# Kernel optimization log

Hardware: AMD Instinct MI355X
Metric: run time of the kernel (lower is better)

The kernel has to match this reference:

```python
import jax, jax.numpy as jnp
import numpy as np

B, S, D, H = 2, 2048, 2048, 16
HD = D // H


def setup_inputs() -> dict:
    key = jax.random.key(0)
    ks = jax.random.split(key, 9)
    s = 1.0 / np.sqrt(D)
    return {
        "hidden_states": jax.random.normal(ks[0], (B, S, D), dtype=jnp.float32),
        "attention_mask": jnp.ones((B, 1, 1, S), dtype=jnp.int32),
        "Wq": jax.random.normal(ks[1], (D, D), dtype=jnp.float32) * s,
        "bq": jnp.zeros((D,), dtype=jnp.float32),
        "Wk": jax.random.normal(ks[2], (D, D), dtype=jnp.float32) * s,
        "bk": jnp.zeros((D,), dtype=jnp.float32),
        "Wv": jax.random.normal(ks[3], (D, D), dtype=jnp.float32) * s,
        "bv": jnp.zeros((D,), dtype=jnp.float32),
        "Wo": jax.random.normal(ks[4], (D, D), dtype=jnp.float32) * s,
        "bo": jnp.zeros((D,), dtype=jnp.float32),
    }


def reference(hidden_states, attention_mask, Wq, bq, Wk, bk, Wv, bv, Wo, bo):
    scale = 1.0 / np.sqrt(HD)
    # projections: torch Linear is x @ W.T + b
    q = hidden_states @ Wq.T + bq
    k = hidden_states @ Wk.T + bk
    v = hidden_states @ Wv.T + bv
    # [B,S,D] -> [B,H,S,hd]
    q = q.reshape(B, S, H, HD).transpose(0, 2, 1, 3)
    k = k.reshape(B, S, H, HD).transpose(0, 2, 1, 3)
    v = v.reshape(B, S, H, HD).transpose(0, 2, 1, 3)
    scores = jnp.einsum("bhqd,bhkd->bhqk", q, k) * scale
    scores = jnp.where(attention_mask == 0, jnp.float32(-1e9), scores)
    probs = jax.nn.softmax(scores, axis=-1)
    attn = jnp.einsum("bhqk,bhkd->bhqd", probs, v)
    attn = attn.transpose(0, 2, 1, 3).reshape(B, S, D)
    out = attn @ Wo.T + bo
    return out
```

## Files before the change

### kernel.cpp

```cpp
#include <hip/hip_runtime.h>
#include <hip/hip_bf16.h>
#include <stdint.h>

typedef __attribute__((ext_vector_type(8))) short short8;
typedef __attribute__((ext_vector_type(8))) unsigned short ushort8;
typedef __attribute__((ext_vector_type(4))) float f32x4;

#define DEVI __device__ __forceinline__

DEVI unsigned short f2bf(float f) {
    union { float f; unsigned int u; } a;
    a.f = f;
    unsigned int u = a.u;
    u += 0x7fffu + ((u >> 16) & 1u);
    return (unsigned short)(u >> 16);
}

DEVI void stage16(const unsigned short* g, unsigned short* ldsbase) {
    __builtin_amdgcn_global_load_lds(
        (const __attribute__((address_space(1))) void*)(uintptr_t)g,
        (__attribute__((address_space(3))) void*)(uintptr_t)ldsbase,
        16, 0, 0);
}

__global__ void cast_all(const float* __restrict__ hs, const float* __restrict__ wq,
                         const float* __restrict__ wk, const float* __restrict__ wv,
                         const float* __restrict__ wo, unsigned short* __restrict__ dst) {
    int i = blockIdx.x * blockDim.x + threadIdx.x;
    const float* src;
    int local;
    if (i < 1048576) { src = hs; local = i; }
    else {
        int j = i - 1048576;
        int w = j >> 19;
        local = j & 524287;
        src = (w == 0) ? wq : (w == 1) ? wk : (w == 2) ? wv : wo;
    }
    const float4* s = (const float4*)src;
    float4 x = s[2 * local], y = s[2 * local + 1];
    ushort8 o;
    o[0] = f2bf(x.x); o[1] = f2bf(x.y); o[2] = f2bf(x.z); o[3] = f2bf(x.w);
    o[4] = f2bf(y.x); o[5] = f2bf(y.y); o[6] = f2bf(y.z); o[7] = f2bf(y.w);
    *(ushort8*)(dst + 8 * i) = o;
}

#define QSCALE 0.12751879523173862f

DEVI void stageg(const unsigned short* gT, unsigned short* ldsTile, int wrow0, int kcol) {
    stage16(gT + wrow0 * 2048 + kcol, ldsTile + wrow0 * 64);
}

__launch_bounds__(512, 2)
__global__ void gemm_qkv(const unsigned short* __restrict__ A, const unsigned short* __restrict__ Bstack,
                         const float* __restrict__ bq, const float* __restrict__ bk,
                         const float* __restrict__ bv, unsigned short* __restrict__ qb,
                         unsigned short* __restrict__ kb, unsigned short* __restrict__ vtb) {
    constexpr int K = 2048, NT = 32;
    __shared__ __align__(16) unsigned short As[2][16384];
    __shared__ __align__(16) unsigned short Bs[2][16384];
    const int tid = threadIdx.x;
    const int lane = tid & 63, wid = tid >> 6;
    const int quad = lane >> 4, l15 = lane & 15;
    const int m0 = blockIdx.y * 256, n0 = blockIdx.x * 256;
    const int mode = n0 >> 11;
    const int wm = (wid & 1) * 128, wn = (wid >> 1) * 64;

    const int wa = wid * 8;
    const int wb = (wid >> 2) * 64 + (wid & 3) * 8;
    const int rib = lane >> 3;
    const int cg = (lane & 7) ^ rib;
    const unsigned short* AgT = A + (m0 + rib) * K + cg * 8;
    const unsigned short* BgT = Bstack + (n0 + rib) * K + cg * 8;

    f32x4 acc[8][4];
#pragma unroll
    for (int i = 0; i < 8; i++)
#pragma unroll
        for (int j = 0; j < 4; j++) acc[i][j] = f32x4{0.f, 0.f, 0.f, 0.f};

    stageg(AgT, As[0], wa, 0);       stageg(AgT, As[0], 128 + wa, 0);
    stageg(BgT, Bs[0], wb, 0);       stageg(BgT, Bs[0], 128 + wb, 0);
    stageg(BgT, Bs[0], 32 + wb, 0);  stageg(BgT, Bs[0], 160 + wb, 0);
    stageg(AgT, As[0], 64 + wa, 0);  stageg(AgT, As[0], 192 + wa, 0);
    stageg(AgT, As[1], wa, 64);      stageg(AgT, As[1], 128 + wa, 64);
    stageg(BgT, Bs[1], wb, 64);      stageg(BgT, Bs[1], 128 + wb, 64);
    asm volatile("s_waitcnt vmcnt(4)" ::: "memory");
    __builtin_amdgcn_s_barrier();

    short8 af[4][2], bf0[2][2], bf1[2][2];
    for (int i = 0; i < NT; i++) {
        const int cur = i & 1, nxt = cur ^ 1;
        const unsigned short* Ac = As[cur];
        const unsigned short* Bc = Bs[cur];

#pragma unroll
        for (int mi = 0; mi < 4; mi++) {
            int row = wm + mi * 16 + l15;
#pragma unroll
            for (int kw = 0; kw < 2; kw++) {
                int cc = (kw * 4 + quad) ^ (row & 7);
                af[mi][kw] = *(const short8*)&Ac[row * 64 + cc * 8];
            }
        }
#pragma unroll
        for (int ni = 0; ni < 2; ni++) {
            int row = wn + ni * 16 + l15;
#pragma unroll
            for (int kw = 0; kw < 2; kw++) {
                int cc = (kw * 4 + quad) ^ (row & 7);
                bf0[ni][kw] = *(const short8*)&Bc[row * 64 + cc * 8];
            }
        }
        if (i + 1 < NT) {
            stageg(BgT, Bs[nxt], 32 + wb, (i + 1) * 64);
            stageg(BgT, Bs[nxt], 160 + wb, (i + 1) * 64);
        }
        __builtin_amdgcn_s_barrier();
        asm volatile("s_waitcnt lgkmcnt(0)" ::: "memory");
        __builtin_amdgcn_sched_barrier(0);
        __builtin_amdgcn_s_setprio(1);
#pragma unroll
        for (int kw = 0; kw < 2; kw++)
#pragma unroll
            for (int mi = 0; mi < 4; mi++)
#pragma unroll
                for (int ni = 0; ni < 2; ni++)
                    acc[mi][ni] = __builtin_amdgcn_mfma_f32_16x16x32_bf16(af[mi][kw], bf0[ni][kw], acc[mi][ni], 0, 0, 0);
        __builtin_amdgcn_s_setprio(0);
        __builtin_amdgcn_s_barrier();

#pragma unroll
        for (int ni = 0; ni < 2; ni++) {
            int row = wn + 32 + ni * 16 + l15;
#pragma unroll
            for (int kw = 0; kw < 2; kw++) {
                int cc = (kw * 4 + quad) ^ (row & 7);
                bf1[ni][kw] = *(const short8*)&Bc[row * 64 + cc * 8];
            }
        }
        if (i + 1 < NT) {
            stageg(AgT, As[nxt], 64 + wa, (i + 1) * 64);
            stageg(AgT, As[nxt], 192 + wa, (i + 1) * 64);
        }
        __builtin_amdgcn_s_barrier();
        asm volatile("s_waitcnt lgkmcnt(0)" ::: "memory");
        __builtin_amdgcn_sched_barrier(0);
        __builtin_amdgcn_s_setprio(1);
#pragma unroll
        for (int kw = 0; kw < 2; kw++)
#pragma unroll
            for (int mi = 0; mi < 4; mi++)
#pragma unroll
                for (int ni = 0; ni < 2; ni++)
                    acc[mi][2 + ni] = __builtin_amdgcn_mfma_f32_16x16x32_bf16(af[mi][kw], bf1[ni][kw], acc[mi][2 + ni], 0, 0, 0);
        __builtin_amdgcn_s_setprio(0);
        __builtin_amdgcn_s_barrier();

#pragma unroll
        for (int mi = 0; mi < 4; mi++) {
            int row = wm + 64 + mi * 16 + l15;
#pragma unroll
            for (int kw = 0; kw < 2; kw++) {
                int cc = (kw * 4 + quad) ^ (row & 7);
                af[mi][kw] = *(const short8*)&Ac[row * 64 + cc * 8];
            }
        }
        if (i + 2 < NT) {
            stageg(AgT, As[cur], wa, (i + 2) * 64);
            stageg(AgT, As[cur], 128 + wa, (i + 2) * 64);
        }
        __builtin_amdgcn_s_barrier();
        asm volatile("s_waitcnt lgkmcnt(0)" ::: "memory");
        __builtin_amdgcn_sched_barrier(0);
        __builtin_amdgcn_s_setprio(1);
#pragma unroll
        for (int kw = 0; kw < 2; kw++)
#pragma unroll
            for (int mi = 0; mi < 4; mi++)
#pragma unroll
                for (int ni = 0; ni < 2; ni++)
                    acc[4 + mi][2 + ni] = __builtin_amdgcn_mfma_f32_16x16x32_bf16(af[mi][kw], bf1[ni][kw], acc[4 + mi][2 + ni], 0, 0, 0);
        __builtin_amdgcn_s_setprio(0);
        __builtin_amdgcn_s_barrier();

        if (i + 2 < NT) {
            stageg(BgT, Bs[cur], wb, (i + 2) * 64);
            stageg(BgT, Bs[cur], 128 + wb, (i + 2) * 64);
        }
        if (i < NT - 2) asm volatile("s_waitcnt vmcnt(4)" ::: "memory");
        else            asm volatile("s_waitcnt vmcnt(0)" ::: "memory");
        __builtin_amdgcn_s_barrier();
        __builtin_amdgcn_s_setprio(1);
#pragma unroll
        for (int kw = 0; kw < 2; kw++)
#pragma unroll
            for (int mi = 0; mi < 4; mi++)
#pragma unroll
                for (int ni = 0; ni < 2; ni++)
                    acc[4 + mi][ni] = __builtin_amdgcn_mfma_f32_16x16x32_bf16(af[mi][kw], bf0[ni][kw], acc[4 + mi][ni], 0, 0, 0);
        __builtin_amdgcn_s_setprio(0);
        __builtin_amdgcn_s_barrier();
    }

    const float* bias = (mode == 0) ? bq : (mode == 1) ? bk : bv;
#pragma unroll
    for (int mi = 0; mi < 8; mi++) {
#pragma unroll
        for (int ni = 0; ni < 4; ni++) {
            int n = n0 + wn + ni * 16 + l15;
            int nl = n & 2047;
            float bb = bias[nl];
            if (mode == 2) {
                int m_base = m0 + wm + mi * 16 + quad * 4;
                int h = nl >> 7, dd = nl & 127, bbb = m_base >> 11, s = m_base & 2047;
                unsigned int v0 = f2bf(acc[mi][ni][0] + bb) | ((unsigned int)f2bf(acc[mi][ni][1] + bb) << 16);
                unsigned int v1 = f2bf(acc[mi][ni][2] + bb) | ((unsigned int)f2bf(acc[mi][ni][3] + bb) << 16);
                uint2 pk; pk.x = v0; pk.y = v1;
                *(uint2*)&vtb[((bbb * 16 + h) * 128 + dd) * 2048 + s] = pk;
            } else {
                unsigned short* dst = (mode == 0) ? qb : kb;
                float sc = (mode == 0) ? QSCALE : 1.0f;
#pragma unroll
                for (int r = 0; r < 4; r++) {
                    int m = m0 + wm + mi * 16 + quad * 4 + r;
                    dst[m * 2048 + nl] = f2bf((acc[mi][ni][r] + bb) * sc);
                }
            }
        }
    }
}

__launch_bounds__(256, 2)
__global__ void gemm_out(const unsigned short* __restrict__ A, const unsigned short* __restrict__ Bw,
                         const float* __restrict__ bias, float* __restrict__ Cout) {
    constexpr int K = 2048;
    __shared__ __align__(16) unsigned short As[2 * 4096];
    __shared__ __align__(16) unsigned short Bs[2 * 4096];
    const int tid = threadIdx.x;
    const int lane = tid & 63, wid = tid >> 6;
    const int quad = lane >> 4, l15 = lane & 15;
    const int m0 = blockIdx.y * 128, n0 = blockIdx.x * 128;
    const int wm = (wid & 1) * 64, wn = (wid >> 1) * 64;

    f32x4 acc[4][4];
#pragma unroll
    for (int i = 0; i < 4; i++)
#pragma unroll
        for (int j = 0; j < 4; j++) acc[i][j] = f32x4{0.f, 0.f, 0.f, 0.f};

    const int s0 = wid * 128 + lane, s1 = s0 + 64;
    const int r0 = s0 >> 2, c0 = (s0 & 3) ^ (r0 & 3);
    const int r1 = s1 >> 2, c1 = (s1 & 3) ^ (r1 & 3);
    const int ldsoffA0 = wid * 1024, ldsoffA1 = wid * 1024 + 512;
    const unsigned short* Ag0 = &A[(m0 + r0) * K + c0 * 8];
    const unsigned short* Ag1 = &A[(m0 + r1) * K + c1 * 8];
    const unsigned short* Bg0 = &Bw[(n0 + r0) * K + c0 * 8];
    const unsigned short* Bg1 = &Bw[(n0 + r1) * K + c1 * 8];

    stage16(Ag0, &As[ldsoffA0]);
    stage16(Ag1, &As[ldsoffA1]);
    stage16(Bg0, &Bs[ldsoffA0]);
    stage16(Bg1, &Bs[ldsoffA1]);

    for (int i = 0; i < 64; i++) {
        const int cur = (i & 1) * 4096;
        asm volatile("s_waitcnt vmcnt(0)" ::: "memory");
        __syncthreads();
        if (i < 63) {
            const int nxt = 4096 - cur;
            const int koff = (i + 1) * 32;
            stage16(Ag0 + koff, &As[nxt + ldsoffA0]);
            stage16(Ag1 + koff, &As[nxt + ldsoffA1]);
            stage16(Bg0 + koff, &Bs[nxt + ldsoffA0]);
            stage16(Bg1 + koff, &Bs[nxt + ldsoffA1]);
        }
        short8 af[4], bfr[4];
#pragma unroll
        for (int mi = 0; mi < 4; mi++) {
            int row = wm + mi * 16 + l15;
            int cc = quad ^ (row & 3);
            af[mi] = *(const short8*)&As[cur + row * 32 + cc * 8];
        }
#pragma unroll
        for (int ni = 0; ni < 4; ni++) {
            int row = wn + ni * 16 + l15;
            int cc = quad ^ (row & 3);
            bfr[ni] = *(const short8*)&Bs[cur + row * 32 + cc * 8];
        }
#pragma unroll
        for (int mi = 0; mi < 4; mi++)
#pragma unroll
            for (int ni = 0; ni < 4; ni++)
                acc[mi][ni] = __builtin_amdgcn_mfma_f32_16x16x32_bf16(af[mi], bfr[ni], acc[mi][ni], 0, 0, 0);
    }

#pragma unroll
    for (int mi = 0; mi < 4; mi++) {
#pragma unroll
        for (int ni = 0; ni < 4; ni++) {
            int n = n0 + wn + ni * 16 + l15;
            float bb = bias[n];
#pragma unroll
            for (int r = 0; r < 4; r++) {
                int m = m0 + wm + mi * 16 + quad * 4 + r;
                Cout[m * 2048 + n] = acc[mi][ni][r] + bb;
            }
        }
    }
}

__launch_bounds__(512, 1)
__global__ void attn_fused(const unsigned short* __restrict__ Q, const unsigned short* __restrict__ Kb,
                           const unsigned short* __restrict__ VT, const int* __restrict__ mask,
                           unsigned short* __restrict__ Ob) {
    __shared__ __align__(16) unsigned short Ks[2][64 * 128];
    __shared__ __align__(16) unsigned short Vs[2][128 * 64];
    __shared__ __align__(16) unsigned short Ps[8][32 * 72];
    __shared__ int Ms[2048];

    const int tid = threadIdx.x;
    const int lane = tid & 63, wid = tid >> 6;
    const int quad = lane >> 4, l15 = lane & 15;
    const int qt = blockIdx.x, bh = blockIdx.y;
    const int b = bh >> 4, h = bh & 15;
    const int tok0 = b * 2048 + qt * 256 + wid * 32;

    for (int i = tid; i < 2048; i += 512) Ms[i] = mask[b * 2048 + i];

    short8 aq[2][4];
#pragma unroll
    for (int mi = 0; mi < 2; mi++)
#pragma unroll
        for (int c = 0; c < 4; c++)
            aq[mi][c] = *(const short8*)&Q[(tok0 + mi * 16 + l15) * 2048 + h * 128 + c * 32 + quad * 8];

    f32x4 oacc[2][8];
#pragma unroll
    for (int mi = 0; mi < 2; mi++)
#pragma unroll
        for (int c = 0; c < 8; c++) oacc[mi][c] = f32x4{0.f, 0.f, 0.f, 0.f};
    float lacc[2][4] = {{0.f, 0.f, 0.f, 0.f}, {0.f, 0.f, 0.f, 0.f}};

    const unsigned short* Kbase = Kb + b * 2048 * 2048 + h * 128;
    const unsigned short* Vbase = VT + (b * 16 + h) * 128 * 2048;

    const unsigned short* KgP[2];
    const unsigned short* VgP[2];
    int ldsKoff[2], ldsVoff[2];
#pragma unroll
    for (int j = 0; j < 2; j++) {
        int s = wid * 128 + j * 64 + lane;
        int kr = s >> 4, kc = (s & 15) ^ (kr & 7);
        int vr = s >> 3, vc = (s & 7) ^ (vr & 7);
        KgP[j] = Kbase + kr * 2048 + kc * 8;
        VgP[j] = Vbase + vr * 2048 + vc * 8;
        ldsKoff[j] = (wid * 128 + j * 64) * 8;
        ldsVoff[j] = (wid * 128 + j * 64) * 8;
    }
    unsigned short* pw = &Ps[wid][0];

#pragma unroll
    for (int j = 0; j < 2; j++) {
        stage16(KgP[j], &Ks[0][ldsKoff[j]]);
        stage16(VgP[j], &Vs[0][ldsVoff[j]]);
    }

    for (int kt = 0; kt < 32; kt++) {
        const int cur = kt & 1;
        const int key0 = kt * 64;
        asm volatile("s_waitcnt vmcnt(0)" ::: "memory");
        __syncthreads();
        if (kt < 31) {
            const int nb = cur ^ 1;
            const int key0n = key0 + 64;
#pragma unroll
            for (int j = 0; j < 2; j++) {
                stage16(KgP[j] + key0n * 2048, &Ks[nb][ldsKoff[j]]);
                stage16(VgP[j] + key0n, &Vs[nb][ldsVoff[j]]);
            }
        }
        int mk[4];
#pragma unroll
        for (int t = 0; t < 4; t++) mk[t] = Ms[key0 + t * 16 + l15];

        f32x4 sc[2][4];
#pragma unroll
        for (int mi = 0; mi < 2; mi++)
#pragma unroll
            for (int t = 0; t < 4; t++) sc[mi][t] = f32x4{0.f, 0.f, 0.f, 0.f};
#pragma unroll
        for (int c = 0; c < 4; c++)
#pragma unroll
            for (int t = 0; t < 4; t++) {
                int row = t * 16 + l15;
                int cc = (4 * c + quad) ^ (row & 7);
                short8 bk = *(const short8*)&Ks[cur][row * 128 + cc * 8];
                sc[0][t] = __builtin_amdgcn_mfma_f32_16x16x32_bf16(aq[0][c], bk, sc[0][t], 0, 0, 0);
                sc[1][t] = __builtin_amdgcn_mfma_f32_16x16x32_bf16(aq[1][c], bk, sc[1][t], 0, 0, 0);
            }

#pragma unroll
        for (int mi = 0; mi < 2; mi++)
#pragma unroll
            for (int t = 0; t < 4; t++)
#pragma unroll
                for (int r = 0; r < 4; r++) {
                    float cs = mk[t] ? sc[mi][t][r] : -1e30f;
                    float p = __builtin_amdgcn_exp2f(cs);
                    lacc[mi][r] += p;
                    pw[(mi * 16 + quad * 4 + r) * 72 + t * 16 + l15] = f2bf(p);
                }
        asm volatile("s_waitcnt lgkmcnt(0)" ::: "memory");
        short8 ap[2][2];
#pragma unroll
        for (int mi = 0; mi < 2; mi++)
#pragma unroll
            for (int kk = 0; kk < 2; kk++)
                ap[mi][kk] = *(const short8*)&pw[(mi * 16 + l15) * 72 + kk * 32 + quad * 8];

#pragma unroll
        for (int kk = 0; kk < 2; kk++)
#pragma unroll
            for (int dt = 0; dt < 8; dt++) {
                int row = dt * 16 + l15;
                int cc = (kk * 4 + quad) ^ (row & 7);
                short8 bv = *(const short8*)&Vs[cur][row * 64 + cc * 8];
                oacc[0][dt] = __builtin_amdgcn_mfma_f32_16x16x32_bf16(ap[0][kk], bv, oacc[0][dt], 0, 0, 0);
                oacc[1][dt] = __builtin_amdgcn_mfma_f32_16x16x32_bf16(ap[1][kk], bv, oacc[1][dt], 0, 0, 0);
            }
    }

    float inv[2][4];
#pragma unroll
    for (int mi = 0; mi < 2; mi++)
#pragma unroll
        for (int r = 0; r < 4; r++) {
            float l = lacc[mi][r];
#pragma unroll
            for (int off = 1; off < 16; off <<= 1) l += __shfl_xor(l, off, 64);
            inv[mi][r] = 1.0f / l;
        }
#pragma unroll
    for (int mi = 0; mi < 2; mi++)
#pragma unroll
        for (int dt = 0; dt < 8; dt++)
#pragma unroll
            for (int r = 0; r < 4; r++) {
                float val = oacc[mi][dt][r] * inv[mi][r];
                Ob[(tok0 + mi * 16 + quad * 4 + r) * 2048 + h * 128 + dt * 16 + l15] = f2bf(val);
            }
}

extern "C" void kernel_launch(void* const* d_in, const int* in_sizes, int n_in,
                              void* d_out, int out_size, void* d_ws, size_t ws_size,
                              hipStream_t stream) {
    const float* hs = (const float*)d_in[0];
    const int* mask = (const int*)d_in[1];
    const float* Wq = (const float*)d_in[2];
    const float* bq = (const float*)d_in[3];
    const float* Wk = (const float*)d_in[4];
    const float* bk = (const float*)d_in[5];
    const float* Wv = (const float*)d_in[6];
    const float* bv = (const float*)d_in[7];
    const float* Wo = (const float*)d_in[8];
    const float* bo = (const float*)d_in[9];

    unsigned short* hsb = (unsigned short*)d_ws;
    unsigned short* wqb = hsb + 8388608;
    unsigned short* wob = wqb + 3 * 4194304;
    unsigned short* qb  = wob + 4194304;
    unsigned short* kb  = qb  + 8388608;
    unsigned short* vtb = kb  + 8388608;
    unsigned short* ab  = vtb + 8388608;

    cast_all<<<12288, 256, 0, stream>>>(hs, Wq, Wk, Wv, Wo, hsb);

    gemm_qkv<<<dim3(24, 16), 512, 0, stream>>>(hsb, wqb, bq, bk, bv, qb, kb, vtb);
    attn_fused<<<dim3(8, 32), 512, 0, stream>>>(qb, kb, vtb, mask, ab);
    gemm_out<<<dim3(16, 32), 256, 0, stream>>>(ab, wob, bo, (float*)d_out);
}
```

Measured before the change: 380.8 us.

## Shrink QKV GEMM tile to 256x128 and restructure pipeline to two phases

The QKV projection GEMM drops from 256x256 to 256x128 output tiles, doubling the grid to 768 blocks. Each wave now owns a 64x64 sub-tile, so the inner loop has two MFMA phases instead of four, with new staging and vmcnt wait counts. The smaller tile halves B-tile LDS and accumulator registers, which should help occupancy and wave balance across CUs. In exchange, arithmetic intensity per block drops and the A tile is reloaded by twice as many blocks.

```diff
diff --git a/kernel.cpp b/kernel.cpp
--- a/kernel.cpp
+++ b/kernel.cpp
@@ -57,13 +57,13 @@
                          unsigned short* __restrict__ kb, unsigned short* __restrict__ vtb) {
     constexpr int K = 2048, NT = 32;
     __shared__ __align__(16) unsigned short As[2][16384];
-    __shared__ __align__(16) unsigned short Bs[2][16384];
+    __shared__ __align__(16) unsigned short Bs[2][8192];
     const int tid = threadIdx.x;
     const int lane = tid & 63, wid = tid >> 6;
     const int quad = lane >> 4, l15 = lane & 15;
-    const int m0 = blockIdx.y * 256, n0 = blockIdx.x * 256;
+    const int m0 = blockIdx.y * 256, n0 = blockIdx.x * 128;
     const int mode = n0 >> 11;
-    const int wm = (wid & 1) * 128, wn = (wid >> 1) * 64;
+    const int wm = (wid >> 1) * 64, wn = (wid & 1) * 64;
 
     const int wa = wid * 8;
     const int wb = (wid >> 2) * 64 + (wid & 3) * 8;
@@ -72,19 +72,20 @@
     const unsigned short* AgT = A + (m0 + rib) * K + cg * 8;
     const unsigned short* BgT = Bstack + (n0 + rib) * K + cg * 8;
 
-    f32x4 acc[8][4];
-#pragma unroll
-    for (int i = 0; i < 8; i++)
+    f32x4 acc[4][4];
+#pragma unroll
+    for (int i = 0; i < 4; i++)
 #pragma unroll
         for (int j = 0; j < 4; j++) acc[i][j] = f32x4{0.f, 0.f, 0.f, 0.f};
 
-    stageg(AgT, As[0], wa, 0);       stageg(AgT, As[0], 128 + wa, 0);
-    stageg(BgT, Bs[0], wb, 0);       stageg(BgT, Bs[0], 128 + wb, 0);
-    stageg(BgT, Bs[0], 32 + wb, 0);  stageg(BgT, Bs[0], 160 + wb, 0);
-    stageg(AgT, As[0], 64 + wa, 0);  stageg(AgT, As[0], 192 + wa, 0);
-    stageg(AgT, As[1], wa, 64);      stageg(AgT, As[1], 128 + wa, 64);
-    stageg(BgT, Bs[1], wb, 64);      stageg(BgT, Bs[1], 128 + wb, 64);
-    asm volatile("s_waitcnt vmcnt(4)" ::: "memory");
+    stageg(AgT, As[0], wa, 0);       stageg(AgT, As[0], 64 + wa, 0);
+    stageg(AgT, As[0], 128 + wa, 0); stageg(AgT, As[0], 192 + wa, 0);
+    stageg(BgT, Bs[0], wb, 0);
+    stageg(BgT, Bs[0], 32 + wb, 0);
+    stageg(AgT, As[1], wa, 64);       stageg(AgT, As[1], 64 + wa, 64);
+    stageg(AgT, As[1], 128 + wa, 64); stageg(AgT, As[1], 192 + wa, 64);
+    stageg(BgT, Bs[1], wb, 64);
+    asm volatile("s_waitcnt vmcnt(6)" ::: "memory");
     __builtin_amdgcn_s_barrier();
 
     short8 af[4][2], bf0[2][2], bf1[2][2];
@@ -111,10 +112,9 @@
                 bf0[ni][kw] = *(const short8*)&Bc[row * 64 + cc * 8];
             }
         }
-        if (i + 1 < NT) {
-            stageg(BgT, Bs[nxt], 32 + wb, (i + 1) * 64);
-            stageg(BgT, Bs[nxt], 160 + wb, (i + 1) * 64);
-        }
+        if (i + 1 < NT) stageg(BgT, Bs[nxt], 32 + wb, (i + 1) * 64);
+        if (i < NT - 1) asm volatile("s_waitcnt vmcnt(6)" ::: "memory");
+        else            asm volatile("s_waitcnt vmcnt(0)" ::: "memory");
         __builtin_amdgcn_s_barrier();
         asm volatile("s_waitcnt lgkmcnt(0)" ::: "memory");
         __builtin_amdgcn_sched_barrier(0);
@@ -138,10 +138,15 @@
                 bf1[ni][kw] = *(const short8*)&Bc[row * 64 + cc * 8];
             }
         }
-        if (i + 1 < NT) {
-            stageg(AgT, As[nxt], 64 + wa, (i + 1) * 64);
-            stageg(AgT, As[nxt], 192 + wa, (i + 1) * 64);
-        }
+        if (i + 2 < NT) {
+            const int kc = (i + 2) * 64;
+            stageg(AgT, As[cur], wa, kc);       stageg(AgT, As[cur], 64 + wa, kc);
+            stageg(AgT, As[cur], 128 + wa, kc); stageg(AgT, As[cur], 192 + wa, kc);
+            stageg(BgT, Bs[cur], wb, kc);
+        }
+        if (i < NT - 2)      asm volatile("s_waitcnt vmcnt(6)" ::: "memory");
+        else if (i == NT - 2) asm volatile("s_waitcnt vmcnt(1)" ::: "memory");
+        else                 asm volatile("s_waitcnt vmcnt(0)" ::: "memory");
         __builtin_amdgcn_s_barrier();
         asm volatile("s_waitcnt lgkmcnt(0)" ::: "memory");
         __builtin_amdgcn_sched_barrier(0);
@@ -155,56 +160,11 @@
                     acc[mi][2 + ni] = __builtin_amdgcn_mfma_f32_16x16x32_bf16(af[mi][kw], bf1[ni][kw], acc[mi][2 + ni], 0, 0, 0);
         __builtin_amdgcn_s_setprio(0);
         __builtin_amdgcn_s_barrier();
-
-#pragma unroll
-        for (int mi = 0; mi < 4; mi++) {
-            int row = wm + 64 + mi * 16 + l15;
-#pragma unroll
-            for (int kw = 0; kw < 2; kw++) {
-                int cc = (kw * 4 + quad) ^ (row & 7);
-                af[mi][kw] = *(const short8*)&Ac[row * 64 + cc * 8];
-            }
-        }
-        if (i + 2 < NT) {
-            stageg(AgT, As[cur], wa, (i + 2) * 64);
-            stageg(AgT, As[cur], 128 + wa, (i + 2) * 64);
-        }
-        __builtin_amdgcn_s_barrier();
-        asm volatile("s_waitcnt lgkmcnt(0)" ::: "memory");
-        __builtin_amdgcn_sched_barrier(0);
-        __builtin_amdgcn_s_setprio(1);
-#pragma unroll
-        for (int kw = 0; kw < 2; kw++)
-#pragma unroll
-            for (int mi = 0; mi < 4; mi++)
-#pragma unroll
-                for (int ni = 0; ni < 2; ni++)
-                    acc[4 + mi][2 + ni] = __builtin_amdgcn_mfma_f32_16x16x32_bf16(af[mi][kw], bf1[ni][kw], acc[4 + mi][2 + ni], 0, 0, 0);
-        __builtin_amdgcn_s_setprio(0);
-        __builtin_amdgcn_s_barrier();
-
-        if (i + 2 < NT) {
-            stageg(BgT, Bs[cur], wb, (i + 2) * 64);
-            stageg(BgT, Bs[cur], 128 + wb, (i + 2) * 64);
-        }
-        if (i < NT - 2) asm volatile("s_waitcnt vmcnt(4)" ::: "memory");
-        else            asm volatile("s_waitcnt vmcnt(0)" ::: "memory");
-        __builtin_amdgcn_s_barrier();
-        __builtin_amdgcn_s_setprio(1);
-#pragma unroll
-        for (int kw = 0; kw < 2; kw++)
-#pragma unroll
-            for (int mi = 0; mi < 4; mi++)
-#pragma unroll
-                for (int ni = 0; ni < 2; ni++)
-                    acc[4 + mi][ni] = __builtin_amdgcn_mfma_f32_16x16x32_bf16(af[mi][kw], bf0[ni][kw], acc[4 + mi][ni], 0, 0, 0);
-        __builtin_amdgcn_s_setprio(0);
-        __builtin_amdgcn_s_barrier();
     }
 
     const float* bias = (mode == 0) ? bq : (mode == 1) ? bk : bv;
 #pragma unroll
-    for (int mi = 0; mi < 8; mi++) {
+    for (int mi = 0; mi < 4; mi++) {
 #pragma unroll
         for (int ni = 0; ni < 4; ni++) {
             int n = n0 + wn + ni * 16 + l15;
@@ -475,7 +435,7 @@
 
     cast_all<<<12288, 256, 0, stream>>>(hs, Wq, Wk, Wv, Wo, hsb);
 
-    gemm_qkv<<<dim3(24, 16), 512, 0, stream>>>(hsb, wqb, bq, bk, bv, qb, kb, vtb);
+    gemm_qkv<<<dim3(48, 16), 512, 0, stream>>>(hsb, wqb, bq, bk, bv, qb, kb, vtb);
     attn_fused<<<dim3(8, 32), 512, 0, stream>>>(qb, kb, vtb, mask, ab);
     gemm_out<<<dim3(16, 32), 256, 0, stream>>>(ab, wob, bo, (float*)d_out);
 }
```

Measured after the change: 381.8 us. About the same (+0.3%).
